# Kernel optimization log

Hardware: AMD Instinct MI355X
Metric: run time of the kernel (lower is better)

Reference implementation:

```python
import jax, jax.numpy as jnp
import numpy as np

B, S, HID = 1, 2048, 2048
NH, NKV, HD = 32, 8, 64  # query heads, kv heads, head dim
NEG = -1e9


def rotate_half(x):
    d = x.shape[-1] // 2
    return jnp.concatenate([-x[..., d:], x[..., :d]], axis=-1)


def setup_inputs() -> dict:
    key = jax.random.key(0)
    ks = jax.random.split(key, 8)
    hidden_states = jax.random.normal(ks[0], (B, S, HID), dtype=jnp.float32)
    # RoPE angles: realistic cos/sin tables (B, S, HD)
    inv_freq = 1.0 / (10000.0 ** (np.arange(0, HD, 2, dtype=np.float32) / HD))
    pos = np.arange(S, dtype=np.float32)
    ang = pos[:, None] * inv_freq[None, :]            # (S, HD/2)
    ang = np.concatenate([ang, ang], axis=-1)          # (S, HD)
    cos = jnp.broadcast_to(jnp.cos(ang)[None], (B, S, HD)).astype(jnp.float32)
    sin = jnp.broadcast_to(jnp.sin(ang)[None], (B, S, HD)).astype(jnp.float32)
    # additive causal mask (B, 1, S, S)
    causal = jnp.where(jnp.tril(jnp.ones((S, S), dtype=bool)), 0.0, NEG).astype(jnp.float32)
    attention_mask = jnp.broadcast_to(causal[None, None], (B, 1, S, S))
    std = 0.02
    Wq = jax.random.normal(ks[1], (NH * HD, HID), dtype=jnp.float32) * std
    Wk = jax.random.normal(ks[2], (NKV * HD, HID), dtype=jnp.float32) * std
    Wv = jax.random.normal(ks[3], (NKV * HD, HID), dtype=jnp.float32) * std
    Wo = jax.random.normal(ks[4], (HID, NH * HD), dtype=jnp.float32) * std
    return {"hidden_states": hidden_states, "cos": cos, "sin": sin,
            "attention_mask": attention_mask, "Wq": Wq, "Wk": Wk, "Wv": Wv, "Wo": Wo}


def reference(hidden_states, cos, sin, attention_mask, Wq, Wk, Wv, Wo):
    scaling = HD ** -0.5
    n_rep = NH // NKV
    # projections -> (B, H, S, D)
    q = jnp.einsum('bsh,qh->bsq', hidden_states, Wq).reshape(B, S, NH, HD).transpose(0, 2, 1, 3)
    k = jnp.einsum('bsh,qh->bsq', hidden_states, Wk).reshape(B, S, NKV, HD).transpose(0, 2, 1, 3)
    v = jnp.einsum('bsh,qh->bsq', hidden_states, Wv).reshape(B, S, NKV, HD).transpose(0, 2, 1, 3)
    # RoPE (cos/sin broadcast over head dim via [:, None])
    c, s = cos[:, None], sin[:, None]
    q = q * c + rotate_half(q) * s
    k = k * c + rotate_half(k) * s
    # GQA repeat_kv
    k = jnp.repeat(k, n_rep, axis=1)
    v = jnp.repeat(v, n_rep, axis=1)
    # eager attention
    attn_weights = jnp.einsum('bhqd,bhkd->bhqk', q, k) * scaling
    attn_weights = attn_weights + attention_mask
    attn_weights = jax.nn.softmax(attn_weights.astype(jnp.float32), axis=-1).astype(q.dtype)
    attn_output = jnp.einsum('bhqk,bhkd->bhqd', attn_weights, v)
    attn_output = attn_output.transpose(0, 2, 1, 3).reshape(B, S, NH * HD)
    attn_output = jnp.einsum('bsq,hq->bsh', attn_output, Wo)
    return attn_output, attn_weights
```

## Files before the change

### kernel.cpp

```cpp
#include <hip/hip_runtime.h>

#define S_LEN 2048
#define NH 32
#define NKV 8
#define HD 64
#define QH_DIM (NH * HD)
#define QKV_DIM 3072
#define K_OFF 2048
#define V_OFF 2560
#define LOG2E 1.44269504089f

typedef __attribute__((ext_vector_type(8))) __bf16 bf16x8;
typedef __attribute__((ext_vector_type(4))) float fx4;
typedef __attribute__((ext_vector_type(8))) unsigned short ush8;

__device__ __forceinline__ unsigned short f2bf(float f) {
  return __builtin_bit_cast(unsigned short, (__bf16)f);
}
__device__ __forceinline__ float bf2f(unsigned short h) {
  unsigned int u = ((unsigned int)h) << 16;
  return __builtin_bit_cast(float, u);
}
__device__ __forceinline__ fx4 zero4() {
  fx4 z; z[0] = 0.f; z[1] = 0.f; z[2] = 0.f; z[3] = 0.f; return z;
}

#define MFMA16(a, b, c) __builtin_amdgcn_mfma_f32_16x16x32_bf16((a), (b), (c), 0, 0, 0)

__device__ __forceinline__ void gl16(const void* g, void* l) {
  __builtin_amdgcn_global_load_lds((const __attribute__((address_space(1))) void*)g,
                                   (__attribute__((address_space(3))) void*)l, 16, 0, 0);
}

__global__ __launch_bounds__(256) void cast5(const float* __restrict__ s0, unsigned short* d0, int n0,
                                             const float* __restrict__ s1, unsigned short* d1, int n1,
                                             const float* __restrict__ s2, unsigned short* d2, int n2,
                                             const float* __restrict__ s3, unsigned short* d3, int n3,
                                             const float* __restrict__ s4, unsigned short* d4, int n4) {
  int i = blockIdx.x * 256 + threadIdx.x;
  const float* s;
  unsigned short* d;
  if (i < n0) { s = s0; d = d0; }
  else if ((i -= n0) < n1) { s = s1; d = d1; }
  else if ((i -= n1) < n2) { s = s2; d = d2; }
  else if ((i -= n2) < n3) { s = s3; d = d3; }
  else if ((i -= n3) < n4) { s = s4; d = d4; }
  else return;
  float4 v = ((const float4*)s)[i];
  ushort4 o;
  o.x = f2bf(v.x); o.y = f2bf(v.y); o.z = f2bf(v.z); o.w = f2bf(v.w);
  ((ushort4*)d)[i] = o;
}

__global__ __launch_bounds__(256) void fused_pre(unsigned short* __restrict__ qkv,
                                                 const float* __restrict__ cosp,
                                                 const float* __restrict__ sinp,
                                                 unsigned short* __restrict__ Vt) {
  __shared__ unsigned short t[64][72];
  int b = blockIdx.x;
  if (b < 2560) {
    unsigned short* buf;
    int nheads;
    float scale;
    int idx;
    if (b < 2048) {
      buf = qkv; nheads = NH; scale = 0.125f * LOG2E;
      idx = b * 256 + threadIdx.x;
    } else {
      buf = qkv + K_OFF; nheads = NKV; scale = 1.0f;
      idx = (b - 2048) * 256 + threadIdx.x;
    }
    int j = idx & 7;
    int tt = idx >> 3;
    int head = tt % nheads;
    int s = tt / nheads;
    size_t base = (size_t)s * QKV_DIM + head * 64 + j * 4;
    ushort4 xl = *(const ushort4*)&buf[base];
    ushort4 xh = *(const ushort4*)&buf[base + 32];
    fx4 cl = *(const fx4*)&cosp[s * 64 + j * 4];
    fx4 ch = *(const fx4*)&cosp[s * 64 + 32 + j * 4];
    fx4 sl = *(const fx4*)&sinp[s * 64 + j * 4];
    fx4 sh = *(const fx4*)&sinp[s * 64 + 32 + j * 4];
    ushort4 ol, oh;
    ol.x = f2bf((bf2f(xl.x) * cl[0] - bf2f(xh.x) * sl[0]) * scale);
    ol.y = f2bf((bf2f(xl.y) * cl[1] - bf2f(xh.y) * sl[1]) * scale);
    ol.z = f2bf((bf2f(xl.z) * cl[2] - bf2f(xh.z) * sl[2]) * scale);
    ol.w = f2bf((bf2f(xl.w) * cl[3] - bf2f(xh.w) * sl[3]) * scale);
    oh.x = f2bf((bf2f(xh.x) * ch[0] + bf2f(xl.x) * sh[0]) * scale);
    oh.y = f2bf((bf2f(xh.y) * ch[1] + bf2f(xl.y) * sh[1]) * scale);
    oh.z = f2bf((bf2f(xh.z) * ch[2] + bf2f(xl.z) * sh[2]) * scale);
    oh.w = f2bf((bf2f(xh.w) * ch[3] + bf2f(xl.w) * sh[3]) * scale);
    *(ushort4*)&buf[base] = ol;
    *(ushort4*)&buf[base + 32] = oh;
  } else {
    const unsigned short* V = qkv + V_OFF;
    const int tid = threadIdx.x;
    const int bb = b - 2560;
    const int cb = (bb & 7) * 64;
    const int rb = (bb >> 3) * 64;
#pragma unroll
    for (int rr = 0; rr < 2; rr++) {
      int row = rr * 32 + (tid >> 3);
      int c8 = (tid & 7) * 8;
      *(ush8*)&t[row][c8] = *(const ush8*)&V[(size_t)(rb + row) * QKV_DIM + cb + c8];
    }
    __syncthreads();
#pragma unroll
    for (int rr = 0; rr < 2; rr++) {
      int col = rr * 32 + (tid >> 3);
      int r8 = (tid & 7) * 8;
      ush8 o;
#pragma unroll
      for (int j = 0; j < 8; j++) o[j] = t[r8 + j][col];
      *(ush8*)&Vt[(size_t)(cb + col) * S_LEN + rb + r8] = o;
    }
  }
}

template <int F32OUT>
__global__ __launch_bounds__(512) void gemm_bt(const unsigned short* __restrict__ A,
                                               const unsigned short* __restrict__ B,
                                               void* __restrict__ C, int M, int N, int K) {
  __shared__ unsigned short As[2][128 * 64];
  __shared__ unsigned short Bs[2][128 * 64];
  const int tid = threadIdx.x;
  const int bn = blockIdx.x * 128, bm = blockIdx.y * 128;
  const int lane = tid & 63, wid = tid >> 6;
  const int lo = lane & 15, g = lane >> 4;
  const int wr = wid >> 2, wc = wid & 3;

  fx4 acc[4][2];
#pragma unroll
  for (int i = 0; i < 4; i++)
#pragma unroll
    for (int j = 0; j < 2; j++) acc[i][j] = zero4();

  const int srow = tid >> 3;
  const int cg = (tid & 7) ^ (srow & 7);
  const unsigned short* apg = &A[(size_t)(bm + srow) * K + cg * 8];
  const unsigned short* bpg = &B[(size_t)(bn + srow) * K + cg * 8];
  const size_t istep = (size_t)64 * K;

  const int arow = wr * 64 + lo;
  const int brow = wc * 32 + lo;

#define G_STAGE(s, k0)                              \
  do {                                              \
    gl16(apg + (k0), &As[s][tid * 8]);              \
    gl16(apg + istep + (k0), &As[s][tid * 8 + 4096]); \
    gl16(bpg + (k0), &Bs[s][tid * 8]);              \
    gl16(bpg + istep + (k0), &Bs[s][tid * 8 + 4096]); \
  } while (0)

#define G_COMPUTE(s)                                                        \
  do {                                                                      \
    _Pragma("unroll") for (int ks = 0; ks < 2; ks++) {                      \
      const int sc = ((ks * 4 + g) ^ (lo & 7)) * 8;                         \
      bf16x8 af[4], bb[2];                                                  \
      _Pragma("unroll") for (int mi = 0; mi < 4; mi++)                      \
          af[mi] = *(const bf16x8*)&As[s][(arow + mi * 16) * 64 + sc];      \
      _Pragma("unroll") for (int nj = 0; nj < 2; nj++)                      \
          bb[nj] = *(const bf16x8*)&Bs[s][(brow + nj * 16) * 64 + sc];      \
      _Pragma("unroll") for (int mi = 0; mi < 4; mi++)                      \
          _Pragma("unroll") for (int nj = 0; nj < 2; nj++)                  \
              acc[mi][nj] = MFMA16(af[mi], bb[nj], acc[mi][nj]);            \
    }                                                                       \
  } while (0)

  const int NT = K >> 6;
  G_STAGE(0, 0);
  __syncthreads();
  int cur = 0;
  for (int t = 0; t < NT - 1; ++t) {
    G_STAGE(cur ^ 1, (t + 1) * 64);
    G_COMPUTE(cur);
    __syncthreads();
    cur ^= 1;
  }
  G_COMPUTE(cur);
#undef G_STAGE
#undef G_COMPUTE

#pragma unroll
  for (int mi = 0; mi < 4; mi++)
#pragma unroll
    for (int nj = 0; nj < 2; nj++)
#pragma unroll
      for (int r = 0; r < 4; r++) {
        int row = bm + wr * 64 + mi * 16 + g * 4 + r;
        int col = bn + wc * 32 + nj * 16 + lo;
        if (F32OUT)
          ((float*)C)[(size_t)row * N + col] = acc[mi][nj][r];
        else
          ((unsigned short*)C)[(size_t)row * N + col] = f2bf(acc[mi][nj][r]);
      }
}

__global__ __launch_bounds__(256) void attn_kernel(const unsigned short* __restrict__ Q,
                                                   const unsigned short* __restrict__ Kb,
                                                   const unsigned short* __restrict__ Vt,
                                                   float* __restrict__ P,
                                                   unsigned short* __restrict__ AO) {
  __shared__ unsigned short pls[16][2048];
  __shared__ float lred[4][16];
  const int h = blockIdx.x;
  const int rt = 127 - blockIdx.y;
  const int hkv = h >> 2;
  const int wid = threadIdx.x >> 6, lane = threadIdx.x & 63;
  const int lo = lane & 15, g = lane >> 4;
  const int rowb = rt * 16;
  const int nkt = (rt + 4) >> 2;
  const int qg = rowb + lo;
  char* const plsb = (char*)pls;
  const int swz = (lo & 7) << 4;

  {
    const int zc0 = nkt * 64;
    const int nz4 = (S_LEN - zc0) >> 2;
    for (int idx = threadIdx.x; idx < 16 * nz4; idx += 256) {
      const int r = idx / nz4;
      const int c = idx - r * nz4;
      __builtin_nontemporal_store(zero4(),
          (fx4*)&P[((size_t)h * S_LEN + rowb + r) * S_LEN + zc0 + c * 4]);
    }
  }

  const bf16x8 qa0 = *(const bf16x8*)&Q[(size_t)qg * QKV_DIM + h * HD + g * 8];
  const bf16x8 qa1 = *(const bf16x8*)&Q[(size_t)qg * QKV_DIM + h * HD + 32 + g * 8];

  float l = 0.f;
  {
    bf16x8 kc0[4], kc1[4];
    const int kt0 = wid;
    if (kt0 < nkt) {
#pragma unroll
      for (int nj = 0; nj < 4; nj++) {
        const int kcol = kt0 * 64 + nj * 16 + lo;
        kc0[nj] = *(const bf16x8*)&Kb[(size_t)kcol * QKV_DIM + hkv * HD + g * 8];
        kc1[nj] = *(const bf16x8*)&Kb[(size_t)kcol * QKV_DIM + hkv * HD + 32 + g * 8];
      }
    }
    for (int kt = wid; kt < nkt; kt += 4) {
      bf16x8 kn0[4], kn1[4];
      if (kt + 4 < nkt) {
#pragma unroll
        for (int nj = 0; nj < 4; nj++) {
          const int kcol = (kt + 4) * 64 + nj * 16 + lo;
          kn0[nj] = *(const bf16x8*)&Kb[(size_t)kcol * QKV_DIM + hkv * HD + g * 8];
          kn1[nj] = *(const bf16x8*)&Kb[(size_t)kcol * QKV_DIM + hkv * HD + 32 + g * 8];
        }
      }
      fx4 acc[4];
      __builtin_amdgcn_s_setprio(1);
#pragma unroll
      for (int nj = 0; nj < 4; nj++) {
        acc[nj] = MFMA16(kc0[nj], qa0, zero4());
        acc[nj] = MFMA16(kc1[nj], qa1, acc[nj]);
      }
      __builtin_amdgcn_s_setprio(0);
      const bool diag = (kt == nkt - 1);
#pragma unroll
      for (int nj = 0; nj < 4; nj++) {
        float e0, e1, e2, e3;
        {
          float e[4];
#pragma unroll
          for (int r = 0; r < 4; r++) {
            float v = exp2f(acc[nj][r]);
            if (diag && (kt * 64 + nj * 16 + g * 4 + r > qg)) v = 0.f;
            l += v;
            e[r] = v;
          }
          e0 = e[0]; e1 = e[1]; e2 = e[2]; e3 = e[3];
        }
        unsigned int w0 = (unsigned int)f2bf(e0) | ((unsigned int)f2bf(e1) << 16);
        unsigned int w1 = (unsigned int)f2bf(e2) | ((unsigned int)f2bf(e3) << 16);
        uint2 w; w.x = w0; w.y = w1;
        *(uint2*)(plsb + lo * 4096 + ((kt * 128 + nj * 32 + g * 8) ^ swz)) = w;
      }
#pragma unroll
      for (int j = 0; j < 4; j++) { kc0[j] = kn0[j]; kc1[j] = kn1[j]; }
    }
  }
  l += __shfl_xor(l, 16);
  l += __shfl_xor(l, 32);
  if (lane < 16) lred[wid][lo] = l;

  const unsigned short* const vrow = &Vt[(size_t)(hkv * HD + wid * 16 + lo) * S_LEN];
  bf16x8 vc0 = *(const bf16x8*)&vrow[g * 8];
  bf16x8 vc1 = *(const bf16x8*)&vrow[32 + g * 8];

  __syncthreads();

  fx4 oacc = zero4();
  for (int kt = 0; kt < nkt; ++kt) {
    bf16x8 vn0, vn1;
    if (kt + 1 < nkt) {
      vn0 = *(const bf16x8*)&vrow[(kt + 1) * 64 + g * 8];
      vn1 = *(const bf16x8*)&vrow[(kt + 1) * 64 + 32 + g * 8];
    }
    bf16x8 pa0 = *(const bf16x8*)(plsb + lo * 4096 + ((kt * 128 + g * 16) ^ swz));
    bf16x8 pa1 = *(const bf16x8*)(plsb + lo * 4096 + ((kt * 128 + 64 + g * 16) ^ swz));
    __builtin_amdgcn_s_setprio(1);
    oacc = MFMA16(pa0, vc0, oacc);
    oacc = MFMA16(pa1, vc1, oacc);
    __builtin_amdgcn_s_setprio(0);
    vc0 = vn0; vc1 = vn1;
  }
#pragma unroll
  for (int r = 0; r < 4; r++) {
    const int q = g * 4 + r;
    const float linv = 1.f / (lred[0][q] + lred[1][q] + lred[2][q] + lred[3][q]);
    AO[(size_t)(rowb + q) * QH_DIM + h * HD + wid * 16 + lo] = f2bf(oacc[r] * linv);
  }

  float pinv[4];
#pragma unroll
  for (int it = 0; it < 4; it++) {
    const int rho = it * 4 + g;
    pinv[it] = 1.f / (lred[0][rho] + lred[1][rho] + lred[2][rho] + lred[3][rho]);
  }
  float* const pbase = &P[((size_t)h * S_LEN + rowb) * S_LEN];
  for (int kt = wid; kt < nkt; kt += 4) {
#pragma unroll
    for (int it = 0; it < 4; it++) {
      const int rho = it * 4 + g;
      ushort4 b4 = *(const ushort4*)(plsb + rho * 4096 +
                                     ((kt * 128 + lo * 8) ^ ((rho & 7) << 4)));
      fx4 pv;
      pv[0] = bf2f(b4.x) * pinv[it]; pv[1] = bf2f(b4.y) * pinv[it];
      pv[2] = bf2f(b4.z) * pinv[it]; pv[3] = bf2f(b4.w) * pinv[it];
      __builtin_nontemporal_store(pv,
          (fx4*)&pbase[(size_t)rho * S_LEN + kt * 64 + lo * 4]);
    }
  }
}

extern "C" void kernel_launch(void* const* d_in, const int* in_sizes, int n_in,
                              void* d_out, int out_size, void* d_ws, size_t ws_size,
                              hipStream_t stream) {
  const float* hs = (const float*)d_in[0];
  const float* cosp = (const float*)d_in[1];
  const float* sinp = (const float*)d_in[2];
  const float* Wq = (const float*)d_in[4];
  const float* Wk = (const float*)d_in[5];
  const float* Wv = (const float*)d_in[6];
  const float* Wo = (const float*)d_in[7];

  char* w = (char*)d_ws;
  unsigned short* hs_bf   = (unsigned short*)w; w += (size_t)S_LEN * 2048 * 2;
  unsigned short* wqkv_bf = (unsigned short*)w; w += (size_t)QKV_DIM * 2048 * 2;
  unsigned short* wo_bf   = (unsigned short*)w; w += (size_t)2048 * 2048 * 2;
  unsigned short* qkv_bf  = (unsigned short*)w; w += (size_t)S_LEN * QKV_DIM * 2;
  unsigned short* vt_bf   = (unsigned short*)w; w += (size_t)512 * S_LEN * 2;
  unsigned short* ao_bf   = (unsigned short*)w; w += (size_t)S_LEN * QH_DIM * 2;

  float* out0 = (float*)d_out;
  float* P = out0 + (size_t)S_LEN * QH_DIM;

  cast5<<<14336, 256, 0, stream>>>(hs, hs_bf, 1048576,
                                   Wq, wqkv_bf, 1048576,
                                   Wk, wqkv_bf + (size_t)K_OFF * 2048, 262144,
                                   Wv, wqkv_bf + (size_t)V_OFF * 2048, 262144,
                                   Wo, wo_bf, 1048576);

  gemm_bt<0><<<dim3(QKV_DIM / 128, 16), 512, 0, stream>>>(hs_bf, wqkv_bf, (void*)qkv_bf,
                                                          2048, QKV_DIM, 2048);

  fused_pre<<<2816, 256, 0, stream>>>(qkv_bf, cosp, sinp, vt_bf);

  attn_kernel<<<dim3(NH, 128), 256, 0, stream>>>(qkv_bf, qkv_bf + K_OFF, vt_bf, P, ao_bf);

  gemm_bt<1><<<dim3(16, 16), 512, 0, stream>>>(ao_bf, wo_bf, (void*)out0, 2048, 2048, 2048);
}
```

Measured before the change: 279.9 us.

## Split-K both GEMMs with bf16 partials and fuse combine into RoPE/transpose

Both projection GEMMs now run split-K over two K halves with a 32-wide K tile, writing bf16 partial results. Separate combine kernels sum the partials, with the QKV combine folded into the RoPE/scale and V-transpose pass. The QKV partials are staged in the tail of the attention-probability output buffer before attention overwrites it. The attention kernel also interleaves the probability write-out into the PV loop. The aim is more blocks in flight to fill the GPU and overlapping stores with MFMA, at the cost of extra partial traffic, additional bf16 rounding of partials (including the final fp32 output), and aliasing of the output buffer.

New measurement: 260.4 us. -6.9%, faster.

```diff
diff --git a/kernel.cpp b/kernel.cpp
--- a/kernel.cpp
+++ b/kernel.cpp
@@ -52,48 +52,121 @@
   ((ushort4*)d)[i] = o;
 }
 
-__global__ __launch_bounds__(256) void fused_pre(unsigned short* __restrict__ qkv,
-                                                 const float* __restrict__ cosp,
-                                                 const float* __restrict__ sinp,
-                                                 unsigned short* __restrict__ Vt) {
+__global__ __launch_bounds__(512) void gemm_split(const unsigned short* __restrict__ A,
+                                                  const unsigned short* __restrict__ B,
+                                                  unsigned short* __restrict__ Part,
+                                                  int M, int N, int K) {
+  __shared__ unsigned short As[2][128 * 32];
+  __shared__ unsigned short Bs[2][128 * 32];
+  const int tid = threadIdx.x;
+  const int bn = blockIdx.x * 128, bm = blockIdx.y * 128;
+  const int kslice = blockIdx.z;
+  const int KH = K >> 1;
+  const size_t koff = (size_t)kslice * KH;
+  const int lane = tid & 63, wid = tid >> 6;
+  const int lo = lane & 15, g = lane >> 4;
+  const int wr = wid >> 2, wc = wid & 3;
+
+  fx4 acc[4][2];
+#pragma unroll
+  for (int i = 0; i < 4; i++)
+#pragma unroll
+    for (int j = 0; j < 2; j++) acc[i][j] = zero4();
+
+  const int srow = tid >> 2;
+  const int cg = (tid & 3) ^ ((srow >> 1) & 3);
+  const unsigned short* apg = &A[(size_t)(bm + srow) * K + koff + cg * 8];
+  const unsigned short* bpg = &B[(size_t)(bn + srow) * K + koff + cg * 8];
+
+  const int arow = wr * 64 + lo;
+  const int brow = wc * 32 + lo;
+  const int sc = (g ^ ((lo >> 1) & 3)) * 8;
+
+#define G_STAGE(s, k0)                  \
+  do {                                  \
+    gl16(apg + (k0), &As[s][tid * 8]);  \
+    gl16(bpg + (k0), &Bs[s][tid * 8]);  \
+  } while (0)
+
+#define G_COMPUTE(s)                                                   \
+  do {                                                                 \
+    bf16x8 af[4], bb[2];                                               \
+    _Pragma("unroll") for (int mi = 0; mi < 4; mi++)                   \
+        af[mi] = *(const bf16x8*)&As[s][(arow + mi * 16) * 32 + sc];   \
+    _Pragma("unroll") for (int nj = 0; nj < 2; nj++)                   \
+        bb[nj] = *(const bf16x8*)&Bs[s][(brow + nj * 16) * 32 + sc];   \
+    _Pragma("unroll") for (int mi = 0; mi < 4; mi++)                   \
+        _Pragma("unroll") for (int nj = 0; nj < 2; nj++)               \
+            acc[mi][nj] = MFMA16(af[mi], bb[nj], acc[mi][nj]);         \
+  } while (0)
+
+  const int NT = KH >> 5;
+  G_STAGE(0, 0);
+  __syncthreads();
+  int cur = 0;
+  for (int t = 0; t < NT - 1; ++t) {
+    G_STAGE(cur ^ 1, (t + 1) * 32);
+    G_COMPUTE(cur);
+    __syncthreads();
+    cur ^= 1;
+  }
+  G_COMPUTE(cur);
+#undef G_STAGE
+#undef G_COMPUTE
+
+  unsigned short* const pb = &Part[(size_t)kslice * M * N];
+#pragma unroll
+  for (int mi = 0; mi < 4; mi++)
+#pragma unroll
+    for (int nj = 0; nj < 2; nj++)
+#pragma unroll
+      for (int r = 0; r < 4; r++) {
+        int row = bm + wr * 64 + mi * 16 + g * 4 + r;
+        int col = bn + wc * 32 + nj * 16 + lo;
+        pb[(size_t)row * N + col] = f2bf(acc[mi][nj][r]);
+      }
+}
+
+__global__ __launch_bounds__(256) void combine_qkv(const unsigned short* __restrict__ P0,
+                                                   const unsigned short* __restrict__ P1,
+                                                   unsigned short* __restrict__ qkv,
+                                                   const float* __restrict__ cosp,
+                                                   const float* __restrict__ sinp,
+                                                   unsigned short* __restrict__ Vt) {
   __shared__ unsigned short t[64][72];
-  int b = blockIdx.x;
+  const int b = blockIdx.x;
   if (b < 2560) {
-    unsigned short* buf;
-    int nheads;
-    float scale;
-    int idx;
-    if (b < 2048) {
-      buf = qkv; nheads = NH; scale = 0.125f * LOG2E;
-      idx = b * 256 + threadIdx.x;
-    } else {
-      buf = qkv + K_OFF; nheads = NKV; scale = 1.0f;
-      idx = (b - 2048) * 256 + threadIdx.x;
-    }
+    int idx = b * 256 + threadIdx.x;
     int j = idx & 7;
     int tt = idx >> 3;
-    int head = tt % nheads;
-    int s = tt / nheads;
-    size_t base = (size_t)s * QKV_DIM + head * 64 + j * 4;
-    ushort4 xl = *(const ushort4*)&buf[base];
-    ushort4 xh = *(const ushort4*)&buf[base + 32];
+    int head = tt % 40;
+    int s = tt / 40;
+    const float scale = (head < 32) ? 0.125f * LOG2E : 1.0f;
+    const size_t base = (size_t)s * QKV_DIM + head * 64 + j * 4;
+    ushort4 a0l = *(const ushort4*)&P0[base];
+    ushort4 a1l = *(const ushort4*)&P1[base];
+    ushort4 a0h = *(const ushort4*)&P0[base + 32];
+    ushort4 a1h = *(const ushort4*)&P1[base + 32];
+    float xl0 = bf2f(a0l.x) + bf2f(a1l.x), xl1 = bf2f(a0l.y) + bf2f(a1l.y);
+    float xl2 = bf2f(a0l.z) + bf2f(a1l.z), xl3 = bf2f(a0l.w) + bf2f(a1l.w);
+    float xh0 = bf2f(a0h.x) + bf2f(a1h.x), xh1 = bf2f(a0h.y) + bf2f(a1h.y);
+    float xh2 = bf2f(a0h.z) + bf2f(a1h.z), xh3 = bf2f(a0h.w) + bf2f(a1h.w);
     fx4 cl = *(const fx4*)&cosp[s * 64 + j * 4];
     fx4 ch = *(const fx4*)&cosp[s * 64 + 32 + j * 4];
     fx4 sl = *(const fx4*)&sinp[s * 64 + j * 4];
     fx4 sh = *(const fx4*)&sinp[s * 64 + 32 + j * 4];
     ushort4 ol, oh;
-    ol.x = f2bf((bf2f(xl.x) * cl[0] - bf2f(xh.x) * sl[0]) * scale);
-    ol.y = f2bf((bf2f(xl.y) * cl[1] - bf2f(xh.y) * sl[1]) * scale);
-    ol.z = f2bf((bf2f(xl.z) * cl[2] - bf2f(xh.z) * sl[2]) * scale);
-    ol.w = f2bf((bf2f(xl.w) * cl[3] - bf2f(xh.w) * sl[3]) * scale);
-    oh.x = f2bf((bf2f(xh.x) * ch[0] + bf2f(xl.x) * sh[0]) * scale);
-    oh.y = f2bf((bf2f(xh.y) * ch[1] + bf2f(xl.y) * sh[1]) * scale);
-    oh.z = f2bf((bf2f(xh.z) * ch[2] + bf2f(xl.z) * sh[2]) * scale);
-    oh.w = f2bf((bf2f(xh.w) * ch[3] + bf2f(xl.w) * sh[3]) * scale);
-    *(ushort4*)&buf[base] = ol;
-    *(ushort4*)&buf[base + 32] = oh;
+    ol.x = f2bf((xl0 * cl[0] - xh0 * sl[0]) * scale);
+    ol.y = f2bf((xl1 * cl[1] - xh1 * sl[1]) * scale);
+    ol.z = f2bf((xl2 * cl[2] - xh2 * sl[2]) * scale);
+    ol.w = f2bf((xl3 * cl[3] - xh3 * sl[3]) * scale);
+    oh.x = f2bf((xh0 * ch[0] + xl0 * sh[0]) * scale);
+    oh.y = f2bf((xh1 * ch[1] + xl1 * sh[1]) * scale);
+    oh.z = f2bf((xh2 * ch[2] + xl2 * sh[2]) * scale);
+    oh.w = f2bf((xh3 * ch[3] + xl3 * sh[3]) * scale);
+    *(ushort4*)&qkv[base] = ol;
+    *(ushort4*)&qkv[base + 32] = oh;
   } else {
-    const unsigned short* V = qkv + V_OFF;
     const int tid = threadIdx.x;
     const int bb = b - 2560;
     const int cb = (bb & 7) * 64;
@@ -102,7 +175,13 @@
     for (int rr = 0; rr < 2; rr++) {
       int row = rr * 32 + (tid >> 3);
       int c8 = (tid & 7) * 8;
-      *(ush8*)&t[row][c8] = *(const ush8*)&V[(size_t)(rb + row) * QKV_DIM + cb + c8];
+      const size_t src = (size_t)(rb + row) * QKV_DIM + V_OFF + cb + c8;
+      ush8 a = *(const ush8*)&P0[src];
+      ush8 c = *(const ush8*)&P1[src];
+      ush8 o;
+#pragma unroll
+      for (int j = 0; j < 8; j++) o[j] = f2bf(bf2f(a[j]) + bf2f(c[j]));
+      *(ush8*)&t[row][c8] = o;
     }
     __syncthreads();
 #pragma unroll
@@ -117,83 +196,20 @@
   }
 }
 
-template <int F32OUT>
-__global__ __launch_bounds__(512) void gemm_bt(const unsigned short* __restrict__ A,
-                                               const unsigned short* __restrict__ B,
-                                               void* __restrict__ C, int M, int N, int K) {
-  __shared__ unsigned short As[2][128 * 64];
-  __shared__ unsigned short Bs[2][128 * 64];
-  const int tid = threadIdx.x;
-  const int bn = blockIdx.x * 128, bm = blockIdx.y * 128;
-  const int lane = tid & 63, wid = tid >> 6;
-  const int lo = lane & 15, g = lane >> 4;
-  const int wr = wid >> 2, wc = wid & 3;
-
-  fx4 acc[4][2];
-#pragma unroll
-  for (int i = 0; i < 4; i++)
-#pragma unroll
-    for (int j = 0; j < 2; j++) acc[i][j] = zero4();
-
-  const int srow = tid >> 3;
-  const int cg = (tid & 7) ^ (srow & 7);
-  const unsigned short* apg = &A[(size_t)(bm + srow) * K + cg * 8];
-  const unsigned short* bpg = &B[(size_t)(bn + srow) * K + cg * 8];
-  const size_t istep = (size_t)64 * K;
-
-  const int arow = wr * 64 + lo;
-  const int brow = wc * 32 + lo;
-
-#define G_STAGE(s, k0)                              \
-  do {                                              \
-    gl16(apg + (k0), &As[s][tid * 8]);              \
-    gl16(apg + istep + (k0), &As[s][tid * 8 + 4096]); \
-    gl16(bpg + (k0), &Bs[s][tid * 8]);              \
-    gl16(bpg + istep + (k0), &Bs[s][tid * 8 + 4096]); \
-  } while (0)
-
-#define G_COMPUTE(s)                                                        \
-  do {                                                                      \
-    _Pragma("unroll") for (int ks = 0; ks < 2; ks++) {                      \
-      const int sc = ((ks * 4 + g) ^ (lo & 7)) * 8;                         \
-      bf16x8 af[4], bb[2];                                                  \
-      _Pragma("unroll") for (int mi = 0; mi < 4; mi++)                      \
-          af[mi] = *(const bf16x8*)&As[s][(arow + mi * 16) * 64 + sc];      \
-      _Pragma("unroll") for (int nj = 0; nj < 2; nj++)                      \
-          bb[nj] = *(const bf16x8*)&Bs[s][(brow + nj * 16) * 64 + sc];      \
-      _Pragma("unroll") for (int mi = 0; mi < 4; mi++)                      \
-          _Pragma("unroll") for (int nj = 0; nj < 2; nj++)                  \
-              acc[mi][nj] = MFMA16(af[mi], bb[nj], acc[mi][nj]);            \
-    }                                                                       \
-  } while (0)
-
-  const int NT = K >> 6;
-  G_STAGE(0, 0);
-  __syncthreads();
-  int cur = 0;
-  for (int t = 0; t < NT - 1; ++t) {
-    G_STAGE(cur ^ 1, (t + 1) * 64);
-    G_COMPUTE(cur);
-    __syncthreads();
-    cur ^= 1;
-  }
-  G_COMPUTE(cur);
-#undef G_STAGE
-#undef G_COMPUTE
-
-#pragma unroll
-  for (int mi = 0; mi < 4; mi++)
-#pragma unroll
-    for (int nj = 0; nj < 2; nj++)
-#pragma unroll
-      for (int r = 0; r < 4; r++) {
-        int row = bm + wr * 64 + mi * 16 + g * 4 + r;
-        int col = bn + wc * 32 + nj * 16 + lo;
-        if (F32OUT)
-          ((float*)C)[(size_t)row * N + col] = acc[mi][nj][r];
-        else
-          ((unsigned short*)C)[(size_t)row * N + col] = f2bf(acc[mi][nj][r]);
-      }
+__global__ __launch_bounds__(256) void combine_wo(const unsigned short* __restrict__ P0,
+                                                  const unsigned short* __restrict__ P1,
+                                                  float* __restrict__ out) {
+  const int i = blockIdx.x * 256 + threadIdx.x;
+  const size_t base = (size_t)i * 8;
+  ush8 a = *(const ush8*)&P0[base];
+  ush8 b = *(const ush8*)&P1[base];
+  fx4 o0, o1;
+#pragma unroll
+  for (int j = 0; j < 4; j++) o0[j] = bf2f(a[j]) + bf2f(b[j]);
+#pragma unroll
+  for (int j = 0; j < 4; j++) o1[j] = bf2f(a[4 + j]) + bf2f(b[4 + j]);
+  *(fx4*)&out[base] = o0;
+  *(fx4*)&out[base + 4] = o1;
 }
 
 __global__ __launch_bounds__(256) void attn_kernel(const unsigned short* __restrict__ Q,
@@ -231,11 +247,10 @@
   float l = 0.f;
   {
     bf16x8 kc0[4], kc1[4];
-    const int kt0 = wid;
-    if (kt0 < nkt) {
+    if (wid < nkt) {
 #pragma unroll
       for (int nj = 0; nj < 4; nj++) {
-        const int kcol = kt0 * 64 + nj * 16 + lo;
+        const int kcol = wid * 64 + nj * 16 + lo;
         kc0[nj] = *(const bf16x8*)&Kb[(size_t)kcol * QKV_DIM + hkv * HD + g * 8];
         kc1[nj] = *(const bf16x8*)&Kb[(size_t)kcol * QKV_DIM + hkv * HD + 32 + g * 8];
       }
@@ -261,20 +276,16 @@
       const bool diag = (kt == nkt - 1);
 #pragma unroll
       for (int nj = 0; nj < 4; nj++) {
-        float e0, e1, e2, e3;
-        {
-          float e[4];
-#pragma unroll
-          for (int r = 0; r < 4; r++) {
-            float v = exp2f(acc[nj][r]);
-            if (diag && (kt * 64 + nj * 16 + g * 4 + r > qg)) v = 0.f;
-            l += v;
-            e[r] = v;
-          }
-          e0 = e[0]; e1 = e[1]; e2 = e[2]; e3 = e[3];
+        float e[4];
+#pragma unroll
+        for (int r = 0; r < 4; r++) {
+          float v = exp2f(acc[nj][r]);
+          if (diag && (kt * 64 + nj * 16 + g * 4 + r > qg)) v = 0.f;
+          l += v;
+          e[r] = v;
         }
-        unsigned int w0 = (unsigned int)f2bf(e0) | ((unsigned int)f2bf(e1) << 16);
-        unsigned int w1 = (unsigned int)f2bf(e2) | ((unsigned int)f2bf(e3) << 16);
+        unsigned int w0 = (unsigned int)f2bf(e[0]) | ((unsigned int)f2bf(e[1]) << 16);
+        unsigned int w1 = (unsigned int)f2bf(e[2]) | ((unsigned int)f2bf(e[3]) << 16);
         uint2 w; w.x = w0; w.y = w1;
         *(uint2*)(plsb + lo * 4096 + ((kt * 128 + nj * 32 + g * 8) ^ swz)) = w;
       }
@@ -291,6 +302,14 @@
   bf16x8 vc1 = *(const bf16x8*)&vrow[32 + g * 8];
 
   __syncthreads();
+
+  float pinv[4];
+#pragma unroll
+  for (int it = 0; it < 4; it++) {
+    const int rho = it * 4 + g;
+    pinv[it] = 1.f / (lred[0][rho] + lred[1][rho] + lred[2][rho] + lred[3][rho]);
+  }
+  float* const pbase = &P[((size_t)h * S_LEN + rowb) * S_LEN];
 
   fx4 oacc = zero4();
   for (int kt = 0; kt < nkt; ++kt) {
@@ -305,34 +324,27 @@
     oacc = MFMA16(pa0, vc0, oacc);
     oacc = MFMA16(pa1, vc1, oacc);
     __builtin_amdgcn_s_setprio(0);
+    if ((kt & 3) == wid) {
+#pragma unroll
+      for (int it = 0; it < 4; it++) {
+        const int rho = it * 4 + g;
+        ushort4 b4 = *(const ushort4*)(plsb + rho * 4096 +
+                                       ((kt * 128 + lo * 8) ^ ((rho & 7) << 4)));
+        fx4 pv;
+        pv[0] = bf2f(b4.x) * pinv[it]; pv[1] = bf2f(b4.y) * pinv[it];
+        pv[2] = bf2f(b4.z) * pinv[it]; pv[3] = bf2f(b4.w) * pinv[it];
+        __builtin_nontemporal_store(pv,
+            (fx4*)&pbase[(size_t)rho * S_LEN + kt * 64 + lo * 4]);
+      }
+    }
     vc0 = vn0; vc1 = vn1;
   }
+
 #pragma unroll
   for (int r = 0; r < 4; r++) {
     const int q = g * 4 + r;
     const float linv = 1.f / (lred[0][q] + lred[1][q] + lred[2][q] + lred[3][q]);
     AO[(size_t)(rowb + q) * QH_DIM + h * HD + wid * 16 + lo] = f2bf(oacc[r] * linv);
-  }
-
-  float pinv[4];
-#pragma unroll
-  for (int it = 0; it < 4; it++) {
-    const int rho = it * 4 + g;
-    pinv[it] = 1.f / (lred[0][rho] + lred[1][rho] + lred[2][rho] + lred[3][rho]);
-  }
-  float* const pbase = &P[((size_t)h * S_LEN + rowb) * S_LEN];
-  for (int kt = wid; kt < nkt; kt += 4) {
-#pragma unroll
-    for (int it = 0; it < 4; it++) {
-      const int rho = it * 4 + g;
-      ushort4 b4 = *(const ushort4*)(plsb + rho * 4096 +
-                                     ((kt * 128 + lo * 8) ^ ((rho & 7) << 4)));
-      fx4 pv;
-      pv[0] = bf2f(b4.x) * pinv[it]; pv[1] = bf2f(b4.y) * pinv[it];
-      pv[2] = bf2f(b4.z) * pinv[it]; pv[3] = bf2f(b4.w) * pinv[it];
-      __builtin_nontemporal_store(pv,
-          (fx4*)&pbase[(size_t)rho * S_LEN + kt * 64 + lo * 4]);
-    }
   }
 }
 
@@ -348,15 +360,19 @@
   const float* Wo = (const float*)d_in[7];
 
   char* w = (char*)d_ws;
-  unsigned short* hs_bf   = (unsigned short*)w; w += (size_t)S_LEN * 2048 * 2;
-  unsigned short* wqkv_bf = (unsigned short*)w; w += (size_t)QKV_DIM * 2048 * 2;
-  unsigned short* wo_bf   = (unsigned short*)w; w += (size_t)2048 * 2048 * 2;
-  unsigned short* qkv_bf  = (unsigned short*)w; w += (size_t)S_LEN * QKV_DIM * 2;
-  unsigned short* vt_bf   = (unsigned short*)w; w += (size_t)512 * S_LEN * 2;
-  unsigned short* ao_bf   = (unsigned short*)w; w += (size_t)S_LEN * QH_DIM * 2;
+  unsigned short* wo_bf   = (unsigned short*)(w);
+  unsigned short* ao_bf   = (unsigned short*)(w + (((size_t)9) << 20));
+  unsigned short* hs_bf   = (unsigned short*)(w + (((size_t)18) << 20));
+  unsigned short* wqkv_bf = (unsigned short*)(w + (((size_t)27) << 20));
+  unsigned short* qkv_bf  = (unsigned short*)(w + (((size_t)40) << 20));
+  unsigned short* vt_bf   = (unsigned short*)(w + (((size_t)53) << 20));
+  unsigned short* wop     = hs_bf;
 
   float* out0 = (float*)d_out;
   float* P = out0 + (size_t)S_LEN * QH_DIM;
+  const size_t P_BYTES = (size_t)NH * S_LEN * S_LEN * 4;
+  const size_t QKVP_BYTES = (size_t)2 * S_LEN * QKV_DIM * 2;
+  unsigned short* qkvp = (unsigned short*)((char*)P + P_BYTES - QKVP_BYTES);
 
   cast5<<<14336, 256, 0, stream>>>(hs, hs_bf, 1048576,
                                    Wq, wqkv_bf, 1048576,
@@ -364,12 +380,15 @@
                                    Wv, wqkv_bf + (size_t)V_OFF * 2048, 262144,
                                    Wo, wo_bf, 1048576);
 
-  gemm_bt<0><<<dim3(QKV_DIM / 128, 16), 512, 0, stream>>>(hs_bf, wqkv_bf, (void*)qkv_bf,
-                                                          2048, QKV_DIM, 2048);
-
-  fused_pre<<<2816, 256, 0, stream>>>(qkv_bf, cosp, sinp, vt_bf);
+  gemm_split<<<dim3(QKV_DIM / 128, 16, 2), 512, 0, stream>>>(hs_bf, wqkv_bf, qkvp,
+                                                             2048, QKV_DIM, 2048);
+
+  combine_qkv<<<2816, 256, 0, stream>>>(qkvp, qkvp + (size_t)S_LEN * QKV_DIM,
+                                        qkv_bf, cosp, sinp, vt_bf);
 
   attn_kernel<<<dim3(NH, 128), 256, 0, stream>>>(qkv_bf, qkv_bf + K_OFF, vt_bf, P, ao_bf);
 
-  gemm_bt<1><<<dim3(16, 16), 512, 0, stream>>>(ao_bf, wo_bf, (void*)out0, 2048, 2048, 2048);
-}
+  gemm_split<<<dim3(16, 16, 2), 512, 0, stream>>>(ao_bf, wo_bf, wop, 2048, 2048, 2048);
+
+  combine_wo<<<2048, 256, 0, stream>>>(wop, wop + (size_t)S_LEN * QH_DIM, out0);
+}
```
